# Kernel optimization log

Hardware: AMD Instinct MI355X
Metric: run time of the kernel (lower is better)

Reference implementation:

```python
import jax, jax.numpy as jnp
import numpy as np

N_MOL, E_MOL = 50000, 200000
N_PRO, E_PRO = 100000, 800000


def segment_softmax(e, seg, n):
    # e: [E, H] logits, softmax over edges grouped by target node `seg`
    m = jax.ops.segment_max(e, seg, num_segments=n)
    m = jnp.where(jnp.isfinite(m), m, jnp.zeros_like(m))
    ex = jnp.exp(e - m[seg])
    s = jax.ops.segment_sum(ex, seg, num_segments=n)
    return ex / (s[seg] + 1e-16)


def gat_conv(x, edge_index, W, a_src, a_dst, b, heads, out_ch):
    # torch_geometric GATConv (concat=True, add_self_loops=True, neg slope 0.2, eval mode)
    n = x.shape[0]
    loop = jnp.arange(n, dtype=edge_index.dtype)
    src = jnp.concatenate([edge_index[0], loop])
    dst = jnp.concatenate([edge_index[1], loop])
    h = (x @ W).reshape(n, heads, out_ch)            # [N,H,C]
    alpha_s = jnp.sum(h * a_src, axis=-1)            # [N,H]
    alpha_d = jnp.sum(h * a_dst, axis=-1)            # [N,H]
    e = jax.nn.leaky_relu(alpha_s[src] + alpha_d[dst], 0.2)  # [E,H]
    alpha = segment_softmax(e, dst, n)               # [E,H]
    out = jax.ops.segment_sum(alpha[:, :, None] * h[src], dst, num_segments=n)  # [N,H,C]
    return out.reshape(n, heads * out_ch) + b


def gcn_conv(x, edge_index, edge_weight, W, b):
    # torch_geometric GCNConv with edge_weight (add_self_loops=True, sym norm)
    n = x.shape[0]
    loop = jnp.arange(n, dtype=edge_index.dtype)
    src = jnp.concatenate([edge_index[0], loop])
    dst = jnp.concatenate([edge_index[1], loop])
    w = jnp.concatenate([edge_weight, jnp.ones((n,), x.dtype)])
    deg = jax.ops.segment_sum(w, dst, num_segments=n)
    dinv = jnp.where(deg > 0, deg ** -0.5, jnp.zeros_like(deg))
    norm = dinv[src] * w * dinv[dst]                 # [E]
    h = x @ W                                        # [N,C]
    return jax.ops.segment_sum(norm[:, None] * h[src], dst, num_segments=n) + b


def setup_inputs() -> dict:
    key = jax.random.key(0)
    ks = iter(jax.random.split(key, 32))
    rn = lambda shape, s=0.1: jax.random.normal(next(ks), shape, dtype=jnp.float32) * s
    inp = {
        "mol_x": rn((N_MOL, 78), 1.0),
        "mol_edge_index": jax.random.randint(next(ks), (2, E_MOL), 0, N_MOL, dtype=jnp.int32),
        "pro_x": rn((N_PRO, 33), 1.0),
        "pro_edge_index": jax.random.randint(next(ks), (2, E_PRO), 0, N_PRO, dtype=jnp.int32),
        "pro_edge_weight": jax.random.uniform(next(ks), (E_PRO,), dtype=jnp.float32),
        # mol_conv1: GAT 78->78, heads=2
        "W1": rn((78, 156)), "a_src1": rn((2, 78)), "a_dst1": rn((2, 78)), "b1": jnp.zeros((156,), jnp.float32),
        # mol_conv2: GAT 156->156, heads=2
        "W2": rn((156, 312)), "a_src2": rn((2, 156)), "a_dst2": rn((2, 156)), "b2": jnp.zeros((312,), jnp.float32),
        # mol_conv3: GAT 312->312, heads=1
        "W3": rn((312, 312)), "a_src3": rn((1, 312)), "a_dst3": rn((1, 312)), "b3": jnp.zeros((312,), jnp.float32),
        # pro_conv1: GCN 33->33
        "Wp1": rn((33, 33)), "bp1": jnp.zeros((33,), jnp.float32),
        # pro_conv2: GAT 33->66, heads=2
        "Wp2": rn((33, 132)), "ap_src2": rn((2, 66)), "ap_dst2": rn((2, 66)), "bp2": jnp.zeros((132,), jnp.float32),
        # pro_conv3: GAT 132->132, heads=1
        "Wp3": rn((132, 132)), "ap_src3": rn((1, 132)), "ap_dst3": rn((1, 132)), "bp3": jnp.zeros((132,), jnp.float32),
    }
    return inp


def reference(mol_x, mol_edge_index, pro_x, pro_edge_index, pro_edge_weight,
              W1, a_src1, a_dst1, b1, W2, a_src2, a_dst2, b2, W3, a_src3, a_dst3, b3,
              Wp1, bp1, Wp2, ap_src2, ap_dst2, bp2, Wp3, ap_src3, ap_dst3, bp3):
    # mol branch (per CPI_GAT.forward): conv1 -> relu -> conv2 -> relu -> conv3
    x = jax.nn.relu(gat_conv(mol_x, mol_edge_index, W1, a_src1, a_dst1, b1, 2, 78))
    x = jax.nn.relu(gat_conv(x, mol_edge_index, W2, a_src2, a_dst2, b2, 2, 156))
    x = gat_conv(x, mol_edge_index, W3, a_src3, a_dst3, b3, 1, 312)
    # pro branch: gcn -> relu -> gat -> relu -> gat -> relu
    xt = jax.nn.relu(gcn_conv(pro_x, pro_edge_index, pro_edge_weight, Wp1, bp1))
    xt = jax.nn.relu(gat_conv(xt, pro_edge_index, Wp2, ap_src2, ap_dst2, bp2, 2, 66))
    xt = jax.nn.relu(gat_conv(xt, pro_edge_index, Wp3, ap_src3, ap_dst3, bp3, 1, 132))
    return (x, xt)
```

## Files before the change

### kernel.cpp

```cpp
#include <hip/hip_runtime.h>
#include <cstdint>
#include <cstddef>

#define WAVE 64
#define NPB 4

#define TBM 128
#define TBN 128
#define TBK 32
#define LDK 40

typedef short s16x8 __attribute__((ext_vector_type(8)));
typedef float f32x4 __attribute__((ext_vector_type(4)));

__device__ __forceinline__ unsigned short f2bf(float f) {
    unsigned int u = __float_as_uint(f);
    unsigned int r = (u + 0x7fffu + ((u >> 16) & 1u)) >> 16;
    return (unsigned short)r;
}
__device__ __forceinline__ float bf2f_lo(unsigned int v) { return __uint_as_float(v << 16); }
__device__ __forceinline__ float bf2f_hi(unsigned int v) { return __uint_as_float(v & 0xffff0000u); }
__device__ __forceinline__ float lrelu02(float e) { return (e > 0.f) ? e : 0.2f * e; }


__device__ __forceinline__ void gemm_body(const unsigned short* __restrict__ A,
                                          const unsigned short* __restrict__ BT,
                                          unsigned short* __restrict__ Cbf,
                                          float* __restrict__ asb, float* __restrict__ adb,
                                          int N, int Kp, int M, int Mext, int Mp, int H,
                                          int bx, int by) {
    __shared__ __align__(16) unsigned short As[TBM * LDK];
    __shared__ __align__(16) unsigned short Bs[TBN * LDK];
    int tid = threadIdx.x;
    int wave = tid >> 6;
    int lane = tid & 63;
    int rowBase = by * TBM;
    int colBase = bx * TBN;
    int wm = (wave & 1) * 64;
    int wn = (wave >> 1) * 64;
    int l15 = lane & 15;
    int quad = lane >> 4;

    f32x4 acc[4][4];
    f32x4 z4 = {0.f, 0.f, 0.f, 0.f};
#pragma unroll
    for (int i = 0; i < 4; i++)
#pragma unroll
        for (int j = 0; j < 4; j++) acc[i][j] = z4;

    int srow = tid >> 2;
    int skg = tid & 3;
    const uint4 zero16 = {0u, 0u, 0u, 0u};

    for (int k0 = 0; k0 < Kp; k0 += TBK) {
#pragma unroll
        for (int half = 0; half < 2; half++) {
            int row = srow + half * 64;
            int gk = k0 + skg * 8;
            bool kok = (gk < Kp);
            {
                int gr = rowBase + row;
                uint4 v = zero16;
                if (kok && gr < N) v = *(const uint4*)(A + (size_t)gr * Kp + gk);
                *(uint4*)(As + row * LDK + skg * 8) = v;
            }
            {
                int gc = colBase + row;
                uint4 v = zero16;
                if (kok && gc < Mext) v = *(const uint4*)(BT + (size_t)gc * Kp + gk);
                *(uint4*)(Bs + row * LDK + skg * 8) = v;
            }
        }
        __syncthreads();

        s16x8 af[4], bfr[4];
#pragma unroll
        for (int mt = 0; mt < 4; mt++)
            af[mt] = *(const s16x8*)(As + (wm + mt * 16 + l15) * LDK + quad * 8);
#pragma unroll
        for (int nt = 0; nt < 4; nt++)
            bfr[nt] = *(const s16x8*)(Bs + (wn + nt * 16 + l15) * LDK + quad * 8);
#pragma unroll
        for (int mt = 0; mt < 4; mt++)
#pragma unroll
            for (int nt = 0; nt < 4; nt++)
                acc[mt][nt] = __builtin_amdgcn_mfma_f32_16x16x32_bf16(af[mt], bfr[nt], acc[mt][nt], 0, 0, 0);
        __syncthreads();
    }

#pragma unroll
    for (int mt = 0; mt < 4; mt++) {
#pragma unroll
        for (int r = 0; r < 4; r++) {
            int row = rowBase + wm + mt * 16 + quad * 4 + r;
            if (row < N) {
#pragma unroll
                for (int nt = 0; nt < 4; nt++) {
                    int col = colBase + wn + nt * 16 + l15;
                    float v = acc[mt][nt][r];
                    if (col < M) {
                        Cbf[(size_t)row * Mp + col] = f2bf(v);
                    } else if (asb != nullptr && col < M + 2 * H) {
                        int t = col - M;
                        if (t < H) asb[(size_t)row * H + t] = v;
                        else adb[(size_t)row * H + (t - H)] = v;
                    }
                }
            }
        }
    }
}


template <int SLOTS, int G, int H, bool SM, int SWEEPS, bool GCN>
__device__ __forceinline__ void agg_body(const unsigned short* __restrict__ hfeat,
                                         const float* __restrict__ as_, const float* __restrict__ ad_,
                                         const float* __restrict__ dinv,
                                         const int* __restrict__ rowp, const int2* __restrict__ cpack,
                                         const float* __restrict__ bias,
                                         float* __restrict__ out_f, unsigned short* __restrict__ out_bf,
                                         int HC, int ldo, int relu, int n, int lane) {
    constexpr int ROWB = SWEEPS * SLOTS * 16;
    int g = lane / SLOTS;
    int slot = lane - g * SLOTS;
    bool act = (g < G);
    int C = HC / H;
    int beg = rowp[n], end = rowp[n + 1];

    float adn[H], msub[H];
    float di = 0.f;
    if (GCN) {
        di = dinv[n];
    } else {
#pragma unroll
        for (int h = 0; h < H; h++) {
            adn[h] = ad_[(size_t)n * H + h];
            msub[h] = lrelu02(as_[(size_t)n * H + h] + adn[h]);
        }
    }

    int ch0[SWEEPS];
    bool h1q[SWEEPS][4];
#pragma unroll
    for (int sw = 0; sw < SWEEPS; sw++) {
        ch0[sw] = (sw * SLOTS + slot) * 8;
#pragma unroll
        for (int q = 0; q < 4; q++) h1q[sw][q] = (H == 2) && ((ch0[sw] + 2 * q) >= C);
    }

    float sfw = GCN ? di * di : 1.f;
    float accx[SWEEPS][4], accy[SWEEPS][4];
#pragma unroll
    for (int sw = 0; sw < SWEEPS; sw++)
#pragma unroll
        for (int q = 0; q < 4; q++) { accx[sw][q] = 0.f; accy[sw][q] = 0.f; }
    if (act && g == 0) {
#pragma unroll
        for (int sw = 0; sw < SWEEPS; sw++) {
            uint4 v = *(const uint4*)((const char*)hfeat + (size_t)n * ROWB + (sw * SLOTS + slot) * 16);
            unsigned int vv[4] = {v.x, v.y, v.z, v.w};
#pragma unroll
            for (int q = 0; q < 4; q++) { accx[sw][q] = sfw * bf2f_lo(vv[q]); accy[sw][q] = sfw * bf2f_hi(vv[q]); }
        }
    }

    float wsum[H];
#pragma unroll
    for (int h = 0; h < H; h++) wsum[h] = 0.f;

    for (int base = beg; base < end; base += WAVE) {
        int cnt = end - base;
        if (cnt > WAVE) cnt = WAVE;
        int s_l = 0;
// ... 80 lines not shown
                        unsigned int ub[4] = {vB[sw].x, vB[sw].y, vB[sw].z, vB[sw].w};
#pragma unroll
                        for (int q = 0; q < 4; q++) {
                            float wq = (H == 2) ? (h1q[sw][q] ? wB[1] : wB[0]) : wB[0];
                            accx[sw][q] += wq * bf2f_lo(ub[q]);
                            accy[sw][q] += wq * bf2f_hi(ub[q]);
                        }
                    }
                }
            }
        }
    }

    if (G == 3) {
#pragma unroll
        for (int sw = 0; sw < SWEEPS; sw++)
#pragma unroll
            for (int q = 0; q < 4; q++) {
                int b1a = (lane + SLOTS) << 2, b2a = (lane + 2 * SLOTS) << 2;
                float t1 = __uint_as_float((unsigned)__builtin_amdgcn_ds_bpermute(b1a, (int)__float_as_uint(accx[sw][q])));
                float t2 = __uint_as_float((unsigned)__builtin_amdgcn_ds_bpermute(b2a, (int)__float_as_uint(accx[sw][q])));
                accx[sw][q] += t1 + t2;
                float t3 = __uint_as_float((unsigned)__builtin_amdgcn_ds_bpermute(b1a, (int)__float_as_uint(accy[sw][q])));
                float t4 = __uint_as_float((unsigned)__builtin_amdgcn_ds_bpermute(b2a, (int)__float_as_uint(accy[sw][q])));
                accy[sw][q] += t3 + t4;
            }
    } else if (G == 8) {
#pragma unroll
        for (int st = 4; st >= 1; st >>= 1) {
            int ba = (lane + st * SLOTS) << 2;
#pragma unroll
            for (int sw = 0; sw < SWEEPS; sw++)
#pragma unroll
                for (int q = 0; q < 4; q++) {
                    accx[sw][q] += __uint_as_float((unsigned)__builtin_amdgcn_ds_bpermute(ba, (int)__float_as_uint(accx[sw][q])));
                    accy[sw][q] += __uint_as_float((unsigned)__builtin_amdgcn_ds_bpermute(ba, (int)__float_as_uint(accy[sw][q])));
                }
        }
    }

    float rs[H];
    if (SM) {
#pragma unroll
        for (int h = 0; h < H; h++) {
            float t = wsum[h];
            for (int off = 32; off > 0; off >>= 1) t += __shfl_xor(t, off);
            rs[h] = 1.f / (1.f + t + 1e-16f);
        }
    } else {
#pragma unroll
        for (int h = 0; h < H; h++) rs[h] = 1.f;
    }

    if (lane < SLOTS) {
#pragma unroll
        for (int sw = 0; sw < SWEEPS; sw++) {
            float o[8];
#pragma unroll
            for (int q = 0; q < 4; q++) {
                float r = (H == 2) ? (h1q[sw][q] ? rs[1] : rs[0]) : rs[0];
                int c0 = ch0[sw] + 2 * q;
                float b0 = (c0 < HC) ? bias[c0] : 0.f;
                float b1v = (c0 + 1 < HC) ? bias[c0 + 1] : 0.f;
                float o0 = accx[sw][q] * r + b0;
                float o1 = accy[sw][q] * r + b1v;
                if (relu) { o0 = fmaxf(o0, 0.f); o1 = fmaxf(o1, 0.f); }
                if (c0 >= HC) o0 = 0.f;
                if (c0 + 1 >= HC) o1 = 0.f;
                o[2 * q] = o0;
                o[2 * q + 1] = o1;
            }
            if (out_bf) {
                uint4 pk;
                unsigned* pp = (unsigned*)&pk;
#pragma unroll
                for (int q = 0; q < 4; q++)
                    pp[q] = (unsigned)f2bf(o[2 * q]) | ((unsigned)f2bf(o[2 * q + 1]) << 16);
                *(uint4*)((char*)out_bf + (size_t)n * ((size_t)ldo * 2) + (sw * SLOTS + slot) * 16) = pk;
            } else {
#pragma unroll
                for (int half = 0; half < 2; half++) {
                    int c0 = ch0[sw] + half * 4;
                    if (c0 < HC) {
                        float4 f4 = make_float4(o[half * 4], o[half * 4 + 1], o[half * 4 + 2], o[half * 4 + 3]);
                        *(float4*)(out_f + (size_t)n * HC + c0) = f4;
                    }
                }
            }
        }
    }
}


__device__ __forceinline__ void cvtw1(const float* __restrict__ W, unsigned short* __restrict__ WT,
                                      int K, int M, int Kp, int i) {
    int m = i / Kp;
    int k = i - m * Kp;
    WT[i] = (k < K) ? f2bf(W[(long long)k * M + m]) : (unsigned short)0;
}

__device__ __forceinline__ void prep1(const float* __restrict__ W, const float* __restrict__ a_src,
                                      const float* __restrict__ a_dst, unsigned short* __restrict__ WT,
                                      int K, int M, int C, int Kp, int H, int b, int lane) {
    int k = b % Kp;
    int th = b / Kp;
    int t = th / H;
    int h = th - t * H;
    size_t orow = (size_t)(M + t * H + h) * Kp;
    if (k >= K) {
        if (lane == 0) WT[orow + k] = 0;
        return;
    }
    const float* a = t ? a_dst : a_src;
    int hoff = h * C;
    const float* wrow = W + (size_t)k * M + hoff;
    float acc = 0.f;
    for (int c = lane; c < C; c += 64) acc += wrow[c] * a[hoff + c];
    for (int off = 32; off > 0; off >>= 1) acc += __shfl_down(acc, off);
    if (lane == 0) WT[orow + k] = f2bf(acc);
}


__global__ __launch_bounds__(256) void k_A(
    const int* __restrict__ mol_dst, const int* __restrict__ pro_dst, int* __restrict__ cnt,
    int N_MOL, int E_MOL, int ET, int nb1,
    const float* __restrict__ W1, const float* __restrict__ W2, const float* __restrict__ W3,
    const float* __restrict__ Wp1, const float* __restrict__ Wp2, const float* __restrict__ Wp3,
    unsigned short* __restrict__ wt1, unsigned short* __restrict__ wt2, unsigned short* __restrict__ wt3,
    unsigned short* __restrict__ wtp1, unsigned short* __restrict__ wtp2, unsigned short* __restrict__ wtp3,
    const float* __restrict__ as1, const float* __restrict__ ad1,
    const float* __restrict__ as2, const float* __restrict__ ad2,
    const float* __restrict__ as3, const float* __restrict__ ad3,
    const float* __restrict__ aps2, const float* __restrict__ apd2,
    const float* __restrict__ aps3, const float* __restrict__ apd3,
    const float* __restrict__ mol_x, unsigned short* __restrict__ xb,
    const float* __restrict__ pro_x, unsigned short* __restrict__ xpp,
    long long totM, long long totP) {
    const int nb2 = 730;
    const int nb3 = 508;
    int b = blockIdx.x;
    int tid = threadIdx.x;
    if (b < nb1) {
        int i0 = b * 1024 + tid;
#pragma unroll
        for (int k = 0; k < 4; k++) {
            int e = i0 + k * 256;
            if (e < ET) {
                int d = (e < E_MOL) ? mol_dst[e] : (N_MOL + pro_dst[e - E_MOL]);
                atomicAdd(&cnt[d], 1);
            }
        }
    } else if (b < nb1 + nb2) {
        int idx = (b - nb1) * 256 + tid;
        if (idx < 12480)        cvtw1(W1, wt1, 78, 156, 80, idx);
        else if (idx < 62400)   cvtw1(W2, wt2, 156, 312, 160, idx - 12480);
        else if (idx < 162240)  cvtw1(W3, wt3, 312, 312, 320, idx - 62400);
        else if (idx < 163560)  cvtw1(Wp1, wtp1, 33, 33, 40, idx - 162240);
        else if (idx < 168840)  cvtw1(Wp2, wtp2, 33, 132, 40, idx - 163560);
        else if (idx < 186792)  cvtw1(Wp3, wtp3, 132, 132, 136, idx - 168840);
    } else if (b < nb1 + nb2 + nb3) {
        int unit = (b - nb1 - nb2) * 4 + (tid >> 6);
        int lane = tid & 63;
        if (unit < 320)        prep1(W1, as1, ad1, wt1, 78, 156, 78, 80, 2, unit, lane);
        else if (unit < 960)   prep1(W2, as2, ad2, wt2, 156, 312, 156, 160, 2, unit - 320, lane);
        else if (unit < 1600)  prep1(W3, as3, ad3, wt3, 312, 312, 312, 320, 1, unit - 960, lane);
        else if (unit < 1760)  prep1(Wp2, aps2, apd2, wtp2, 33, 132, 66, 40, 2, unit - 1600, lane);
        else if (unit < 2032)  prep1(Wp3, aps3, apd3, wtp3, 132, 132, 132, 136, 1, unit - 1760, lane);
    } else {
        long long i0 = (long long)(b - nb1 - nb2 - nb3) * 1024 + tid;
#pragma unroll
        for (int k = 0; k < 4; k++) {
            long long idx = i0 + k * 256;
            if (idx < totM) {
                int n = (int)(idx / 80);
                int kk = (int)(idx - (long long)n * 80);
                xb[idx] = (kk < 78) ? f2bf(mol_x[(long long)n * 78 + kk]) : (unsigned short)0;
            } else if (idx < totM + totP) {
                long long i2 = idx - totM;
                int n = (int)(i2 / 40);
                int kk = (int)(i2 - (long long)n * 40);
                xpp[i2] = (kk < 33) ? f2bf(pro_x[(long long)n * 33 + kk]) : (unsigned short)0;
            }
        }
    }
}


__global__ __launch_bounds__(256) void k_scan1(const int* __restrict__ cnt, int* __restrict__ incl,
                                               int* __restrict__ bsums, int n) {
    __shared__ int sm[256];
    int i = blockIdx.x * 256 + threadIdx.x;
    int v = (i < n) ? cnt[i] : 0;
    sm[threadIdx.x] = v;
    __syncthreads();
    for (int off = 1; off < 256; off <<= 1) {
        int t = (threadIdx.x >= off) ? sm[threadIdx.x - off] : 0;
        __syncthreads();
        sm[threadIdx.x] += t;
        __syncthreads();
    }
    if (i < n) incl[i] = sm[threadIdx.x];
    if (threadIdx.x == 255) bsums[blockIdx.x] = sm[255];
}

__global__ __launch_bounds__(1024) void k_scan2(int* __restrict__ bsums, int nb) {
    __shared__ int sm[1024];
    int v = (threadIdx.x < nb) ? bsums[threadIdx.x] : 0;
    sm[threadIdx.x] = v;
    __syncthreads();
    for (int off = 1; off < 1024; off <<= 1) {
        int t = (threadIdx.x >= off) ? sm[threadIdx.x - off] : 0;
        __syncthreads();
        sm[threadIdx.x] += t;
        __syncthreads();
    }
    if (threadIdx.x < nb) bsums[threadIdx.x] = sm[threadIdx.x] - v;
}

__global__ __launch_bounds__(256) void k_scan3_all(const int* __restrict__ incl, const int* __restrict__ cnt,
                                                   const int* __restrict__ boff,
                                                   int* __restrict__ mol_rowp, int* __restrict__ pro_rowp,
                                                   int* __restrict__ cur,
                                                   int N_MOL, int N_PRO, int E_MOL, int E_PRO) {
    int i = blockIdx.x * 256 + threadIdx.x;
    int NT = N_MOL + N_PRO;
    if (i < NT) {
        int ex = incl[i] - cnt[i] + boff[blockIdx.x];
        cur[i] = ex;
        if (i < N_MOL) mol_rowp[i] = ex;
        else pro_rowp[i - N_MOL] = ex - E_MOL;
    }
    if (i == 0) {
        mol_rowp[N_MOL] = E_MOL;
        pro_rowp[N_PRO] = E_PRO;
    }
}


__global__ __launch_bounds__(256) void k_B(
    const int* __restrict__ msrc, const int* __restrict__ mdst,
    const int* __restrict__ psrc, const int* __restrict__ pdst,
    const float* __restrict__ pw, int* __restrict__ cur, int2* __restrict__ cpack,
    int N_MOL, int E_MOL, int ET, int nbs,
    const unsigned short* __restrict__ A1, const unsigned short* __restrict__ B1,
    unsigned short* __restrict__ C1, float* __restrict__ as1o, float* __restrict__ ad1o,
    int N1, int Kp1, int M1, int Mext1, int Mp1, int H1, int g1x, int nb1,
    const unsigned short* __restrict__ A2, const unsigned short* __restrict__ B2,
    unsigned short* __restrict__ C2, float* __restrict__ as2o, float* __restrict__ ad2o,
    int N2, int Kp2, int M2, int Mext2, int Mp2, int H2, int g2x) {
    int b = blockIdx.x;
    if (b < nbs) {
        int e = b * 256 + threadIdx.x;
        if (e < ET) {
            int s, d;
            int wbits = 0;
            if (e >= E_MOL) {
                int ep = e - E_MOL;
                s = psrc[ep];
                d = N_MOL + pdst[ep];
                wbits = __float_as_int(pw[ep]);
            } else {
                s = msrc[e];
                d = mdst[e];
            }
            int pos = atomicAdd(&cur[d], 1);
            int2 pk;
            pk.x = s;
            pk.y = wbits;
            cpack[pos] = pk;
        }
    } else if (b < nbs + nb1) {
        int bb = b - nbs;
        gemm_body(A1, B1, C1, as1o, ad1o, N1, Kp1, M1, Mext1, Mp1, H1, bb % g1x, bb / g1x);
    } else {
        int bb = b - nbs - nb1;
        gemm_body(A2, B2, C2, as2o, ad2o, N2, Kp2, M2, Mext2, Mp2, H2, bb % g2x, bb / g2x);
    }
}


__global__ __launch_bounds__(256) void k_deg(const int* __restrict__ rowp, const int2* __restrict__ cpack,
                                             float* __restrict__ dinv, int N) {
    int n = blockIdx.x * 256 + threadIdx.x;
    if (n < N) {
        int b = rowp[n], e = rowp[n + 1];
        float s = 0.f;
        for (int p = b; p < e; p++) s += __int_as_float(cpack[p].y);
        dinv[n] = rsqrtf(s + 1.0f);
    }
}


__global__ __launch_bounds__(NPB * 64) void k_fuse1(
    const unsigned short* __restrict__ hb, const float* __restrict__ asm_, const float* __restrict__ adm_,
    const int* __restrict__ mrowp, const int2* __restrict__ mcp, const float* __restrict__ b1,
    unsigned short* __restrict__ xb, int Nm,
    const unsigned short* __restrict__ hbp, const float* __restrict__ dinv,
    const int* __restrict__ prowp, const int2* __restrict__ pcp, const float* __restrict__ bp1,
    unsigned short* __restrict__ xpp, int Np, int nb1) {
    int wave = threadIdx.x >> 6, lane = threadIdx.x & 63;
    int b = blockIdx.x;
    if (b < nb1) {
        int n = b * NPB + wave;
        if (n < Nm)
            agg_body<20, 3, 2, true, 1, false>(hb, asm_, adm_, nullptr, mrowp, mcp, b1,
                                               nullptr, xb, 156, 160, 1, n, lane);
    } else {
        int n = (b - nb1) * NPB + wave;
        if (n < Np)
            agg_body<5, 8, 1, false, 1, true>(hbp, nullptr, nullptr, dinv, prowp, pcp, bp1,
                                              nullptr, xpp, 33, 40, 1, n, lane);
    }
}

__global__ __launch_bounds__(NPB * 64) void k_fuse3(
    const unsigned short* __restrict__ hb, const float* __restrict__ asm_, const float* __restrict__ adm_,
    const int* __restrict__ mrowp, const int2* __restrict__ mcp, const float* __restrict__ b2,
    unsigned short* __restrict__ xb, int Nm,
    const unsigned short* __restrict__ hbp, const float* __restrict__ asp_, const float* __restrict__ adp_,
    const int* __restrict__ prowp, const int2* __restrict__ pcp, const float* __restrict__ bp2,
    unsigned short* __restrict__ xpp, int Np, int nb1) {
    int wave = threadIdx.x >> 6, lane = threadIdx.x & 63;
    int b = blockIdx.x;
    if (b < nb1) {
        int n = b * NPB + wave;
        if (n < Nm)
            agg_body<20, 3, 2, true, 2, false>(hb, asm_, adm_, nullptr, mrowp, mcp, b2,
                                               nullptr, xb, 312, 320, 1, n, lane);
    } else {
        int n = (b - nb1) * NPB + wave;
        if (n < Np)
            agg_body<17, 3, 2, true, 1, false>(hbp, asp_, adp_, nullptr, prowp, pcp, bp2,
                                               nullptr, xpp, 132, 136, 1, n, lane);
    }
}

__global__ __launch_bounds__(NPB * 64) void k_fuse5(
    const unsigned short* __restrict__ hb, const float* __restrict__ asm_, const float* __restrict__ adm_,
    const int* __restrict__ mrowp, const int2* __restrict__ mcp, const float* __restrict__ b3,
    float* __restrict__ out_mol, int Nm,
    const unsigned short* __restrict__ hbp, const float* __restrict__ asp_, const float* __restrict__ adp_,
    const int* __restrict__ prowp, const int2* __restrict__ pcp, const float* __restrict__ bp3,
    float* __restrict__ out_pro, int Np, int nb1) {
    int wave = threadIdx.x >> 6, lane = threadIdx.x & 63;
    int b = blockIdx.x;
    if (b < nb1) {
        int n = b * NPB + wave;
        if (n < Nm)
            agg_body<20, 3, 1, true, 2, false>(hb, asm_, adm_, nullptr, mrowp, mcp, b3,
                                               out_mol, nullptr, 312, 320, 0, n, lane);
    } else {
        int n = (b - nb1) * NPB + wave;
        if (n < Np)
            agg_body<17, 3, 1, true, 1, false>(hbp, asp_, adp_, nullptr, prowp, pcp, bp3,
                                               out_pro, nullptr, 132, 136, 1, n, lane);
    }
}


extern "C" void kernel_launch(void* const* d_in, const int* in_sizes, int n_in,
                              void* d_out, int out_size, void* d_ws, size_t ws_size,
                              hipStream_t stream) {
    const int N_MOL = in_sizes[0] / 78;
    const int E_MOL = in_sizes[1] / 2;
    const int N_PRO = in_sizes[2] / 33;
    const int E_PRO = in_sizes[3] / 2;
    const int NT = N_MOL + N_PRO;
    const int ET = E_MOL + E_PRO;

    const float* mol_x = (const float*)d_in[0];
    const int* mol_ei = (const int*)d_in[1];
    const float* pro_x = (const float*)d_in[2];
    const int* pro_ei = (const int*)d_in[3];
    const float* pro_ew = (const float*)d_in[4];
    const float *W1 = (const float*)d_in[5], *as1 = (const float*)d_in[6], *ad1 = (const float*)d_in[7],
                *b1 = (const float*)d_in[8];
    const float *W2 = (const float*)d_in[9], *as2 = (const float*)d_in[10], *ad2 = (const float*)d_in[11],
                *b2 = (const float*)d_in[12];
    const float *W3 = (const float*)d_in[13], *as3 = (const float*)d_in[14], *ad3 = (const float*)d_in[15],
                *b3 = (const float*)d_in[16];
    const float *Wp1 = (const float*)d_in[17], *bp1 = (const float*)d_in[18];
    const float *Wp2 = (const float*)d_in[19], *aps2 = (const float*)d_in[20], *apd2 = (const float*)d_in[21],
                *bp2 = (const float*)d_in[22];
    const float *Wp3 = (const float*)d_in[23], *aps3 = (const float*)d_in[24], *apd3 = (const float*)d_in[25],
                *bp3 = (const float*)d_in[26];

    float* out_mol = (float*)d_out;
    float* out_pro = (float*)d_out + (size_t)N_MOL * 312;

    char* p = (char*)d_ws;
    auto alloc = [&](size_t bytes) -> void* {
        void* r = (void*)p;
        p += (bytes + 255) & ~(size_t)255;
        return r;
    };
    int* cnt_all  = (int*)alloc((size_t)NT * 4);
    int* incl     = (int*)alloc((size_t)NT * 4);
    int* cur_all  = (int*)alloc((size_t)NT * 4);
    int* bsums    = (int*)alloc(1024 * 4);
    int* mol_rowp = (int*)alloc((size_t)(N_MOL + 1) * 4);
    int* pro_rowp = (int*)alloc((size_t)(N_PRO + 1) * 4);
    int2* cpack   = (int2*)alloc((size_t)ET * 8);
    float* dinv   = (float*)alloc((size_t)N_PRO * 4);
    float* asb_m = (float*)alloc((size_t)N_MOL * 2 * 4);
    float* adb_m = (float*)alloc((size_t)N_MOL * 2 * 4);
    float* asb_p = (float*)alloc((size_t)N_PRO * 2 * 4);
    float* adb_p = (float*)alloc((size_t)N_PRO * 2 * 4);
    unsigned short* hb  = (unsigned short*)alloc((size_t)N_MOL * 320 * 2);
    unsigned short* xb  = (unsigned short*)alloc((size_t)N_MOL * 320 * 2);
    unsigned short* hbp = (unsigned short*)alloc((size_t)N_PRO * 136 * 2);
    unsigned short* xpp = (unsigned short*)alloc((size_t)N_PRO * 136 * 2);
    unsigned short* wt1 = (unsigned short*)alloc((size_t)160 * 80 * 2);
    unsigned short* wt2 = (unsigned short*)alloc((size_t)320 * 160 * 2);
    unsigned short* wt3 = (unsigned short*)alloc((size_t)320 * 320 * 2);
    unsigned short* wtp1 = (unsigned short*)alloc((size_t)40 * 40 * 2);
    unsigned short* wtp2 = (unsigned short*)alloc((size_t)136 * 40 * 2);
    unsigned short* wtp3 = (unsigned short*)alloc((size_t)136 * 136 * 2);
    (void)ws_size;

    int2* mol_cp = cpack;
    int2* pro_cp = cpack + E_MOL;

    const int* mol_src = mol_ei;
    const int* mol_dst = mol_ei + E_MOL;
    const int* pro_src = pro_ei;
    const int* pro_dst = pro_ei + E_PRO;

    const long long totM = (long long)N_MOL * 80;
    const long long totP = (long long)N_PRO * 40;

    hipMemsetAsync(cnt_all, 0, (size_t)NT * 4, stream);
    int nbCnt = (ET + 1023) / 1024;
    int nbCvx = (int)((totM + totP + 1023) / 1024);
    int gridA = nbCnt + 730 + 508 + nbCvx;
    k_A<<<gridA, 256, 0, stream>>>(mol_dst, pro_dst, cnt_all, N_MOL, E_MOL, ET, nbCnt,
                                   W1, W2, W3, Wp1, Wp2, Wp3, wt1, wt2, wt3, wtp1, wtp2, wtp3,
                                   as1, ad1, as2, ad2, as3, ad3, aps2, apd2, aps3, apd3,
                                   mol_x, xb, pro_x, xpp, totM, totP);

    int nbT = (NT + 255) / 256;
    k_scan1<<<nbT, 256, 0, stream>>>(cnt_all, incl, bsums, NT);
    k_scan2<<<1, 1024, 0, stream>>>(bsums, nbT);
    k_scan3_all<<<nbT, 256, 0, stream>>>(incl, cnt_all, bsums, mol_rowp, pro_rowp, cur_all,
                                         N_MOL, N_PRO, E_MOL, E_PRO);

    int gyM = (N_MOL + TBM - 1) / TBM;
    int gyP = (N_PRO + TBM - 1) / TBM;

    {
        int nbs = (ET + 255) / 256;
        int g1x = (160 + TBN - 1) / TBN;
        int nb1 = g1x * gyM;
        int g2x = 1;
        int nb2 = g2x * gyP;
        k_B<<<nbs + nb1 + nb2, 256, 0, stream>>>(
            mol_src, mol_dst, pro_src, pro_dst, pro_ew, cur_all, cpack, N_MOL, E_MOL, ET, nbs,
            xb, wt1, hb, asb_m, adb_m, N_MOL, 80, 156, 160, 160, 2, g1x, nb1,
            xpp, wtp1, hbp, nullptr, nullptr, N_PRO, 40, 33, 33, 40, 0, g2x);
    }

    k_deg<<<(N_PRO + 255) / 256, 256, 0, stream>>>(pro_rowp, pro_cp, dinv, N_PRO);

    {
        int nb1 = (N_MOL + NPB - 1) / NPB;
        int nb2 = (N_PRO + NPB - 1) / NPB;
        k_fuse1<<<nb1 + nb2, NPB * 64, 0, stream>>>(hb, asb_m, adb_m, mol_rowp, mol_cp, b1, xb, N_MOL,
                                                    hbp, dinv, pro_rowp, pro_cp, bp1, xpp, N_PRO, nb1);
    }

    {
        int g1x = (316 + TBN - 1) / TBN;
        int nb1 = g1x * gyM;
        int g2x = (136 + TBN - 1) / TBN;
        int nb2 = g2x * gyP;
        k_B<<<nb1 + nb2, 256, 0, stream>>>(
            nullptr, nullptr, nullptr, nullptr, nullptr, nullptr, nullptr, N_MOL, E_MOL, ET, 0,
            xb, wt2, hb, asb_m, adb_m, N_MOL, 160, 312, 316, 320, 2, g1x, nb1,
            xpp, wtp2, hbp, asb_p, adb_p, N_PRO, 40, 132, 136, 136, 2, g2x);
    }

    {
        int nb1 = (N_MOL + NPB - 1) / NPB;
        int nb2 = (N_PRO + NPB - 1) / NPB;
        k_fuse3<<<nb1 + nb2, NPB * 64, 0, stream>>>(hb, asb_m, adb_m, mol_rowp, mol_cp, b2, xb, N_MOL,
                                                    hbp, asb_p, adb_p, pro_rowp, pro_cp, bp2, xpp, N_PRO, nb1);
    }

    {
        int g1x = (314 + TBN - 1) / TBN;
        int nb1 = g1x * gyM;
        int g2x = (134 + TBN - 1) / TBN;
        int nb2 = g2x * gyP;
        k_B<<<nb1 + nb2, 256, 0, stream>>>(
            nullptr, nullptr, nullptr, nullptr, nullptr, nullptr, nullptr, N_MOL, E_MOL, ET, 0,
            xb, wt3, hb, asb_m, adb_m, N_MOL, 320, 312, 314, 320, 1, g1x, nb1,
            xpp, wtp3, hbp, asb_p, adb_p, N_PRO, 136, 132, 134, 136, 1, g2x);
    }

    {
        int nb1 = (N_MOL + NPB - 1) / NPB;
        int nb2 = (N_PRO + NPB - 1) / NPB;
        k_fuse5<<<nb1 + nb2, NPB * 64, 0, stream>>>(hb, asb_m, adb_m, mol_rowp, mol_cp, b3, out_mol, N_MOL,
                                                    hbp, asb_p, adb_p, pro_rowp, pro_cp, bp3, out_pro, N_PRO, nb1);
    }
}
```

Before: 764.7 us.

## Aggregate before transform for layer-2 GAT using block-diagonal weights

```diff
diff --git a/kernel.cpp b/kernel.cpp
--- a/kernel.cpp
+++ b/kernel.cpp
@@ -27,6 +27,7 @@
                                           const unsigned short* __restrict__ BT,
                                           unsigned short* __restrict__ Cbf,
                                           float* __restrict__ asb, float* __restrict__ adb,
+                                          const float* __restrict__ bias, int relu, int zpadTo,
                                           int N, int Kp, int M, int Mext, int Mp, int H,
                                           int bx, int by) {
     __shared__ __align__(16) unsigned short As[TBM * LDK];
@@ -99,7 +100,14 @@
                     int col = colBase + wn + nt * 16 + l15;
                     float v = acc[mt][nt][r];
                     if (col < M) {
-                        Cbf[(size_t)row * Mp + col] = f2bf(v);
+                        float v2 = v;
+                        if (bias != nullptr) {
+                            v2 += bias[col];
+                            if (relu) v2 = fmaxf(v2, 0.f);
+                        }
+                        Cbf[(size_t)row * Mp + col] = f2bf(v2);
+                    } else if (col < zpadTo) {
+                        Cbf[(size_t)row * Mp + col] = 0;
                     } else if (asb != nullptr && col < M + 2 * H) {
                         int t = col - M;
                         if (t < H) asb[(size_t)row * H + t] = v;
@@ -112,13 +120,15 @@
 }
 
 
-template <int SLOTS, int G, int H, bool SM, int SWEEPS, bool GCN>
+template <int SLOTS, int G, int H, bool SM, int SWEEPS, bool GCN, bool NEXTA>
 __device__ __forceinline__ void agg_body(const unsigned short* __restrict__ hfeat,
                                          const float* __restrict__ as_, const float* __restrict__ ad_,
                                          const float* __restrict__ dinv,
                                          const int* __restrict__ rowp, const int2* __restrict__ cpack,
                                          const float* __restrict__ bias,
                                          float* __restrict__ out_f, unsigned short* __restrict__ out_bf,
+                                         const float* __restrict__ vanf, int vald,
+                                         float* __restrict__ asn, float* __restrict__ adn_o,
                                          int HC, int ldo, int relu, int n, int lane) {
     constexpr int ROWB = SWEEPS * SLOTS * 16;
     int g = lane / SLOTS;
@@ -305,6 +315,7 @@
         for (int h = 0; h < H; h++) rs[h] = 1.f;
     }
 
+    float ps[4] = {0.f, 0.f, 0.f, 0.f};
     if (lane < SLOTS) {
 #pragma unroll
         for (int sw = 0; sw < SWEEPS; sw++) {
@@ -323,6 +334,14 @@
                 o[2 * q] = o0;
                 o[2 * q + 1] = o1;
             }
+            if (NEXTA) {
+#pragma unroll
+                for (int j = 0; j < 8; j++) {
+                    int c = ch0[sw] + j;
+#pragma unroll
+                    for (int th = 0; th < 4; th++) ps[th] += o[j] * vanf[th * vald + c];
+                }
+            }
             if (out_bf) {
                 uint4 pk;
                 unsigned* pp = (unsigned*)&pk;
@@ -342,6 +361,175 @@
             }
         }
     }
+    if (NEXTA) {
+#pragma unroll
+        for (int th = 0; th < 4; th++)
+            for (int off = 32; off > 0; off >>= 1) ps[th] += __shfl_xor(ps[th], off);
+        if (lane == 0) {
+            asn[(size_t)n * 2 + 0] = ps[0];
+            asn[(size_t)n * 2 + 1] = ps[1];
+            adn_o[(size_t)n * 2 + 0] = ps[2];
+            adn_o[(size_t)n * 2 + 1] = ps[3];
+        }
+    }
+}
+
+
+template <int SLOTS, int G>
+__device__ __forceinline__ void aggN_body(const unsigned short* __restrict__ x,
+                                          const float* __restrict__ as_, const float* __restrict__ ad_,
+                                          const int* __restrict__ rowp, const int2* __restrict__ cpack,
+                                          unsigned short* __restrict__ A2, int n, int lane) {
+    constexpr int ROWB = SLOTS * 16;
+    int g = lane / SLOTS;
+    int slot = lane - g * SLOTS;
+    bool act = (g < G);
+    int beg = rowp[n], end = rowp[n + 1];
+
+    float adn[2], msub[2];
+#pragma unroll
+    for (int h = 0; h < 2; h++) {
+        adn[h] = ad_[(size_t)n * 2 + h];
+        msub[h] = lrelu02(as_[(size_t)n * 2 + h] + adn[h]);
+    }
+
+    float ax[2][4], ay[2][4];
+#pragma unroll
+    for (int h = 0; h < 2; h++)
+#pragma unroll
+        for (int q = 0; q < 4; q++) { ax[h][q] = 0.f; ay[h][q] = 0.f; }
+    if (act && g == 0) {
+        uint4 v = *(const uint4*)((const char*)x + (size_t)n * ROWB + slot * 16);
+        unsigned int vv[4] = {v.x, v.y, v.z, v.w};
+#pragma unroll
+        for (int q = 0; q < 4; q++) {
+            float lo = bf2f_lo(vv[q]), hi = bf2f_hi(vv[q]);
+            ax[0][q] = lo; ax[1][q] = lo;
+            ay[0][q] = hi; ay[1][q] = hi;
+        }
+    }
+
+    float wsum[2] = {0.f, 0.f};
+
+    for (int base = beg; base < end; base += WAVE) {
+        int cnt = end - base;
+        if (cnt > WAVE) cnt = WAVE;
+        int s_l = 0;
+        float w_l[2] = {0.f, 0.f};
+        if (lane < cnt) {
+            s_l = cpack[base + lane].x;
+#pragma unroll
+            for (int h = 0; h < 2; h++)
+                w_l[h] = __expf(lrelu02(as_[(size_t)s_l * 2 + h] + adn[h]) - msub[h]);
+            wsum[0] += w_l[0];
+            wsum[1] += w_l[1];
+        }
+        for (int j0 = 0; j0 < cnt; j0 += 2 * G) {
+            int sA;
+            float wA[2];
+            uint4 vA;
+            {
+                int jj = j0 + g;
+                bool pad = (jj >= cnt);
+                if (jj > cnt - 1) jj = cnt - 1;
+                int ba = jj << 2;
+                sA = __builtin_amdgcn_ds_bpermute(ba, s_l);
+#pragma unroll
+                for (int h = 0; h < 2; h++) {
+                    float t = __uint_as_float(
+                        (unsigned)__builtin_amdgcn_ds_bpermute(ba, (int)__float_as_uint(w_l[h])));
+                    wA[h] = pad ? 0.f : t;
+                }
+                if (act) vA = *(const uint4*)((const char*)x + (unsigned)sA * ROWB + slot * 16);
+            }
+            bool haveB = (j0 + G < cnt);
+            int sB;
+            float wB[2];
+            uint4 vB;
+            if (haveB) {
+                int jj = j0 + G + g;
+                bool pad = (jj >= cnt);
+                if (jj > cnt - 1) jj = cnt - 1;
+                int ba = jj << 2;
+                sB = __builtin_amdgcn_ds_bpermute(ba, s_l);
+#pragma unroll
+                for (int h = 0; h < 2; h++) {
+                    float t = __uint_as_float(
+                        (unsigned)__builtin_amdgcn_ds_bpermute(ba, (int)__float_as_uint(w_l[h])));
+                    wB[h] = pad ? 0.f : t;
+                }
+                if (act) vB = *(const uint4*)((const char*)x + (unsigned)sB * ROWB + slot * 16);
+            }
+            if (act) {
+                unsigned int va[4] = {vA.x, vA.y, vA.z, vA.w};
+#pragma unroll
+                for (int q = 0; q < 4; q++) {
+                    float lo = bf2f_lo(va[q]), hi = bf2f_hi(va[q]);
+                    ax[0][q] += wA[0] * lo; ax[1][q] += wA[1] * lo;
+                    ay[0][q] += wA[0] * hi; ay[1][q] += wA[1] * hi;
+                }
+                if (haveB) {
+                    unsigned int ub[4] = {vB.x, vB.y, vB.z, vB.w};
+#pragma unroll
+                    for (int q = 0; q < 4; q++) {
+                        float lo = bf2f_lo(ub[q]), hi = bf2f_hi(ub[q]);
+                        ax[0][q] += wB[0] * lo; ax[1][q] += wB[1] * lo;
+                        ay[0][q] += wB[0] * hi; ay[1][q] += wB[1] * hi;
+                    }
+                }
+            }
+        }
+    }
+
+    if (G == 3) {
+#pragma unroll
+        for (int h = 0; h < 2; h++)
+#pragma unroll
+            for (int q = 0; q < 4; q++) {
+                int b1a = (lane + SLOTS) << 2, b2a = (lane + 2 * SLOTS) << 2;
+                float t1 = __uint_as_float((unsigned)__builtin_amdgcn_ds_bpermute(b1a, (int)__float_as_uint(ax[h][q])));
+                float t2 = __uint_as_float((unsigned)__builtin_amdgcn_ds_bpermute(b2a, (int)__float_as_uint(ax[h][q])));
+                ax[h][q] += t1 + t2;
+                float t3 = __uint_as_float((unsigned)__builtin_amdgcn_ds_bpermute(b1a, (int)__float_as_uint(ay[h][q])));
+                float t4 = __uint_as_float((unsigned)__builtin_amdgcn_ds_bpermute(b2a, (int)__float_as_uint(ay[h][q])));
+                ay[h][q] += t3 + t4;
+            }
+    } else if (G == 8) {
+#pragma unroll
+        for (int st = 4; st >= 1; st >>= 1) {
+            int ba = (lane + st * SLOTS) << 2;
+#pragma unroll
+            for (int h = 0; h < 2; h++)
+#pragma unroll
+                for (int q = 0; q < 4; q++) {
+                    ax[h][q] += __uint_as_float((unsigned)__builtin_amdgcn_ds_bpermute(ba, (int)__float_as_uint(ax[h][q])));
+                    ay[h][q] += __uint_as_float((unsigned)__builtin_amdgcn_ds_bpermute(ba, (int)__float_as_uint(ay[h][q])));
+                }
+        }
+    }
+
+    float rs[2];
+#pragma unroll
+    for (int h = 0; h < 2; h++) {
+        float t = wsum[h];
+        for (int off = 32; off > 0; off >>= 1) t += __shfl_xor(t, off);
+        rs[h] = 1.f / (1.f + t + 1e-16f);
+    }
+
+    if (lane < SLOTS) {
+#pragma unroll
+        for (int h = 0; h < 2; h++) {
+            uint4 pk;
+            unsigned* pp = (unsigned*)&pk;
+#pragma unroll
+            for (int q = 0; q < 4; q++) {
+                float o0 = ax[h][q] * rs[h];
+                float o1 = ay[h][q] * rs[h];
+                pp[q] = (unsigned)f2bf(o0) | ((unsigned)f2bf(o1) << 16);
+            }
+            *(uint4*)((char*)A2 + (size_t)n * (2 * ROWB) + h * ROWB + slot * 16) = pk;
+        }
+    }
 }
 
 
@@ -350,6 +538,19 @@
     int m = i / Kp;
     int k = i - m * Kp;
     WT[i] = (k < K) ? f2bf(W[(long long)k * M + m]) : (unsigned short)0;
+}
+
+__device__ __forceinline__ void cvtw_bd(const float* __restrict__ W, unsigned short* __restrict__ WT,
+                                        int K, int M, int C, int Kp, int Kph, int i) {
+    int m = i / Kp;
+    int k = i - m * Kp;
+    unsigned short v = 0;
+    if (m < M) {
+        int hm = m / C;
+        int kk = k - hm * Kph;
+        if (kk >= 0 && kk < K) v = f2bf(W[(long long)kk * M + m]);
+    }
+    WT[i] = v;
 }
 
 __device__ __forceinline__ void prep1(const float* __restrict__ W, const float* __restrict__ a_src,
@@ -373,23 +574,44 @@
     if (lane == 0) WT[orow + k] = f2bf(acc);
 }
 
+__device__ __forceinline__ void prep1f(const float* __restrict__ W, const float* __restrict__ a_src,
+                                       const float* __restrict__ a_dst, float* __restrict__ fout,
+                                       int K, int M, int C, int Kp, int H, int b, int lane) {
+    int k = b % Kp;
+    int th = b / Kp;
+    int t = th / H;
+    int h = th - t * H;
+    if (k >= K) {
+        if (lane == 0) fout[(size_t)th * Kp + k] = 0.f;
+        return;
+    }
+    const float* a = t ? a_dst : a_src;
+    int hoff = h * C;
+    const float* wrow = W + (size_t)k * M + hoff;
+    float acc = 0.f;
+    for (int c = lane; c < C; c += 64) acc += wrow[c] * a[hoff + c];
+    for (int off = 32; off > 0; off >>= 1) acc += __shfl_down(acc, off);
+    if (lane == 0) fout[(size_t)th * Kp + k] = acc;
+}
+
 
 __global__ __launch_bounds__(256) void k_A(
     const int* __restrict__ mol_dst, const int* __restrict__ pro_dst, int* __restrict__ cnt,
     int N_MOL, int E_MOL, int ET, int nb1,
     const float* __restrict__ W1, const float* __restrict__ W2, const float* __restrict__ W3,
     const float* __restrict__ Wp1, const float* __restrict__ Wp2, const float* __restrict__ Wp3,
-    unsigned short* __restrict__ wt1, unsigned short* __restrict__ wt2, unsigned short* __restrict__ wt3,
-    unsigned short* __restrict__ wtp1, unsigned short* __restrict__ wtp2, unsigned short* __restrict__ wtp3,
+    unsigned short* __restrict__ wt1, unsigned short* __restrict__ wt2bd, unsigned short* __restrict__ wt3,
+    unsigned short* __restrict__ wtp1, unsigned short* __restrict__ wtp2bd, unsigned short* __restrict__ wtp3,
     const float* __restrict__ as1, const float* __restrict__ ad1,
     const float* __restrict__ as2, const float* __restrict__ ad2,
     const float* __restrict__ as3, const float* __restrict__ ad3,
     const float* __restrict__ aps2, const float* __restrict__ apd2,
     const float* __restrict__ aps3, const float* __restrict__ apd3,
+    float* __restrict__ va2f, float* __restrict__ vap2f,
     const float* __restrict__ mol_x, unsigned short* __restrict__ xb,
     const float* __restrict__ pro_x, unsigned short* __restrict__ xpp,
     long long totM, long long totP) {
-    const int nb2 = 730;
+    const int nb2 = 957;
     const int nb3 = 508;
     int b = blockIdx.x;
     int tid = threadIdx.x;
@@ -406,18 +628,18 @@
     } else if (b < nb1 + nb2) {
         int idx = (b - nb1) * 256 + tid;
         if (idx < 12480)        cvtw1(W1, wt1, 78, 156, 80, idx);
-        else if (idx < 62400)   cvtw1(W2, wt2, 156, 312, 160, idx - 12480);
-        else if (idx < 162240)  cvtw1(W3, wt3, 312, 312, 320, idx - 62400);
-        else if (idx < 163560)  cvtw1(Wp1, wtp1, 33, 33, 40, idx - 162240);
-        else if (idx < 168840)  cvtw1(Wp2, wtp2, 33, 132, 40, idx - 163560);
-        else if (idx < 186792)  cvtw1(Wp3, wtp3, 132, 132, 136, idx - 168840);
+        else if (idx < 114880)  cvtw_bd(W2, wt2bd, 156, 312, 156, 320, 160, idx - 12480);
+        else if (idx < 214720)  cvtw1(W3, wt3, 312, 312, 320, idx - 114880);
+        else if (idx < 216040)  cvtw1(Wp1, wtp1, 33, 33, 40, idx - 214720);
+        else if (idx < 226920)  cvtw_bd(Wp2, wtp2bd, 33, 132, 66, 80, 40, idx - 216040);
+        else if (idx < 244872)  cvtw1(Wp3, wtp3, 132, 132, 136, idx - 226920);
     } else if (b < nb1 + nb2 + nb3) {
         int unit = (b - nb1 - nb2) * 4 + (tid >> 6);
         int lane = tid & 63;
         if (unit < 320)        prep1(W1, as1, ad1, wt1, 78, 156, 78, 80, 2, unit, lane);
-        else if (unit < 960)   prep1(W2, as2, ad2, wt2, 156, 312, 156, 160, 2, unit - 320, lane);
+        else if (unit < 960)   prep1f(W2, as2, ad2, va2f, 156, 312, 156, 160, 2, unit - 320, lane);
         else if (unit < 1600)  prep1(W3, as3, ad3, wt3, 312, 312, 312, 320, 1, unit - 960, lane);
-        else if (unit < 1760)  prep1(Wp2, aps2, apd2, wtp2, 33, 132, 66, 40, 2, unit - 1600, lane);
+        else if (unit < 1760)  prep1f(Wp2, aps2, apd2, vap2f, 33, 132, 66, 40, 2, unit - 1600, lane);
         else if (unit < 2032)  prep1(Wp3, aps3, apd3, wtp3, 132, 132, 132, 136, 1, unit - 1760, lane);
     } else {
         long long i0 = (long long)(b - nb1 - nb2 - nb3) * 1024 + tid;
@@ -497,9 +719,11 @@
     int N_MOL, int E_MOL, int ET, int nbs,
     const unsigned short* __restrict__ A1, const unsigned short* __restrict__ B1,
     unsigned short* __restrict__ C1, float* __restrict__ as1o, float* __restrict__ ad1o,
+    const float* __restrict__ bias1, int relu1, int zpad1,
     int N1, int Kp1, int M1, int Mext1, int Mp1, int H1, int g1x, int nb1,
     const unsigned short* __restrict__ A2, const unsigned short* __restrict__ B2,
     unsigned short* __restrict__ C2, float* __restrict__ as2o, float* __restrict__ ad2o,
+    const float* __restrict__ bias2, int relu2, int zpad2,
     int N2, int Kp2, int M2, int Mext2, int Mp2, int H2, int g2x) {
     int b = blockIdx.x;
     if (b < nbs) {
@@ -524,10 +748,10 @@
         }
     } else if (b < nbs + nb1) {
         int bb = b - nbs;
-        gemm_body(A1, B1, C1, as1o, ad1o, N1, Kp1, M1, Mext1, Mp1, H1, bb % g1x, bb / g1x);
+        gemm_body(A1, B1, C1, as1o, ad1o, bias1, relu1, zpad1, N1, Kp1, M1, Mext1, Mp1, H1, bb % g1x, bb / g1x);
     } else {
         int bb = b - nbs - nb1;
-        gemm_body(A2, B2, C2, as2o, ad2o, N2, Kp2, M2, Mext2, Mp2, H2, bb % g2x, bb / g2x);
+        gemm_body(A2, B2, C2, as2o, ad2o, bias2, relu2, zpad2, N2, Kp2, M2, Mext2, Mp2, H2, bb % g2x, bb / g2x);
     }
 }
 
@@ -547,44 +771,43 @@
 __global__ __launch_bounds__(NPB * 64) void k_fuse1(
     const unsigned short* __restrict__ hb, const float* __restrict__ asm_, const float* __restrict__ adm_,
     const int* __restrict__ mrowp, const int2* __restrict__ mcp, const float* __restrict__ b1,
-    unsigned short* __restrict__ xb, int Nm,
+    unsigned short* __restrict__ x2m, const float* __restrict__ va2f,
+    float* __restrict__ asm2, float* __restrict__ adm2, int Nm,
     const unsigned short* __restrict__ hbp, const float* __restrict__ dinv,
     const int* __restrict__ prowp, const int2* __restrict__ pcp, const float* __restrict__ bp1,
-    unsigned short* __restrict__ xpp, int Np, int nb1) {
+    unsigned short* __restrict__ x2p, const float* __restrict__ vap2f,
+    float* __restrict__ asp2, float* __restrict__ adp2, int Np, int nb1) {
     int wave = threadIdx.x >> 6, lane = threadIdx.x & 63;
     int b = blockIdx.x;
     if (b < nb1) {
         int n = b * NPB + wave;
         if (n < Nm)
-            agg_body<20, 3, 2, true, 1, false>(hb, asm_, adm_, nullptr, mrowp, mcp, b1,
-                                               nullptr, xb, 156, 160, 1, n, lane);
+            agg_body<20, 3, 2, true, 1, false, true>(hb, asm_, adm_, nullptr, mrowp, mcp, b1,
+                                                     nullptr, x2m, va2f, 160, asm2, adm2,
+                                                     156, 160, 1, n, lane);
     } else {
         int n = (b - nb1) * NPB + wave;
         if (n < Np)
-            agg_body<5, 8, 1, false, 1, true>(hbp, nullptr, nullptr, dinv, prowp, pcp, bp1,
-                                              nullptr, xpp, 33, 40, 1, n, lane);
-    }
-}
-
-__global__ __launch_bounds__(NPB * 64) void k_fuse3(
-    const unsigned short* __restrict__ hb, const float* __restrict__ asm_, const float* __restrict__ adm_,
-    const int* __restrict__ mrowp, const int2* __restrict__ mcp, const float* __restrict__ b2,
-    unsigned short* __restrict__ xb, int Nm,
-    const unsigned short* __restrict__ hbp, const float* __restrict__ asp_, const float* __restrict__ adp_,
-    const int* __restrict__ prowp, const int2* __restrict__ pcp, const float* __restrict__ bp2,
-    unsigned short* __restrict__ xpp, int Np, int nb1) {
+            agg_body<5, 8, 1, false, 1, true, true>(hbp, nullptr, nullptr, dinv, prowp, pcp, bp1,
+                                                    nullptr, x2p, vap2f, 40, asp2, adp2,
+                                                    33, 40, 1, n, lane);
+    }
+}
+
+__global__ __launch_bounds__(NPB * 64) void k_fuseN(
+    const unsigned short* __restrict__ x2m, const float* __restrict__ asm2, const float* __restrict__ adm2,
+    const int* __restrict__ mrowp, const int2* __restrict__ mcp, unsigned short* __restrict__ xa2m, int Nm,
+    const unsigned short* __restrict__ x2p, const float* __restrict__ asp2, const float* __restrict__ adp2,
+    const int* __restrict__ prowp, const int2* __restrict__ pcp, unsigned short* __restrict__ xa2p, int Np,
+    int nb1) {
     int wave = threadIdx.x >> 6, lane = threadIdx.x & 63;
     int b = blockIdx.x;
     if (b < nb1) {
         int n = b * NPB + wave;
-        if (n < Nm)
-            agg_body<20, 3, 2, true, 2, false>(hb, asm_, adm_, nullptr, mrowp, mcp, b2,
-                                               nullptr, xb, 312, 320, 1, n, lane);
+        if (n < Nm) aggN_body<20, 3>(x2m, asm2, adm2, mrowp, mcp, xa2m, n, lane);
     } else {
         int n = (b - nb1) * NPB + wave;
-        if (n < Np)
-            agg_body<17, 3, 2, true, 1, false>(hbp, asp_, adp_, nullptr, prowp, pcp, bp2,
-                                               nullptr, xpp, 132, 136, 1, n, lane);
+        if (n < Np) aggN_body<5, 8>(x2p, asp2, adp2, prowp, pcp, xa2p, n, lane);
     }
 }
 
@@ -600,13 +823,15 @@
     if (b < nb1) {
         int n = b * NPB + wave;
         if (n < Nm)
-            agg_body<20, 3, 1, true, 2, false>(hb, asm_, adm_, nullptr, mrowp, mcp, b3,
-                                               out_mol, nullptr, 312, 320, 0, n, lane);
+            agg_body<20, 3, 1, true, 2, false, false>(hb, asm_, adm_, nullptr, mrowp, mcp, b3,
+                                                      out_mol, nullptr, nullptr, 0, nullptr, nullptr,
+                                                      312, 320, 0, n, lane);
     } else {
         int n = (b - nb1) * NPB + wave;
         if (n < Np)
-            agg_body<17, 3, 1, true, 1, false>(hbp, asp_, adp_, nullptr, prowp, pcp, bp3,
-                                               out_pro, nullptr, 132, 136, 1, n, lane);
+            agg_body<17, 3, 1, true, 1, false, false>(hbp, asp_, adp_, nullptr, prowp, pcp, bp3,
+                                                      out_pro, nullptr, nullptr, 0, nullptr, nullptr,
+                                                      132, 136, 1, n, lane);
     }
 }
 
@@ -641,6 +866,18 @@
     float* out_mol = (float*)d_out;
     float* out_pro = (float*)d_out + (size_t)N_MOL * 312;
 
+    char* ob = (char*)d_out;
+    size_t o_xa2m = 0;
+    size_t o_xa2p = o_xa2m + (size_t)N_MOL * 320 * 2;
+    size_t o_xb0  = o_xa2p + (size_t)N_PRO * 80 * 2;
+    size_t o_xp0  = o_xb0 + (size_t)N_MOL * 80 * 2;
+    size_t o_xpp  = o_xp0 + (size_t)N_PRO * 40 * 2;
+    unsigned short* xa2m = (unsigned short*)(ob + o_xa2m);
+    unsigned short* xa2p = (unsigned short*)(ob + o_xa2p);
+    unsigned short* xb0  = (unsigned short*)(ob + o_xb0);
+    unsigned short* xp0  = (unsigned short*)(ob + o_xp0);
+    unsigned short* xpp  = (unsigned short*)(ob + o_xpp);
+
     char* p = (char*)d_ws;
     auto alloc = [&](size_t bytes) -> void* {
         void* r = (void*)p;
@@ -655,21 +892,34 @@
     int* pro_rowp = (int*)alloc((size_t)(N_PRO + 1) * 4);
     int2* cpack   = (int2*)alloc((size_t)ET * 8);
     float* dinv   = (float*)alloc((size_t)N_PRO * 4);
-    float* asb_m = (float*)alloc((size_t)N_MOL * 2 * 4);
-    float* adb_m = (float*)alloc((size_t)N_MOL * 2 * 4);
-    float* asb_p = (float*)alloc((size_t)N_PRO * 2 * 4);
-    float* adb_p = (float*)alloc((size_t)N_PRO * 2 * 4);
-    unsigned short* hb  = (unsigned short*)alloc((size_t)N_MOL * 320 * 2);
-    unsigned short* xb  = (unsigned short*)alloc((size_t)N_MOL * 320 * 2);
-    unsigned short* hbp = (unsigned short*)alloc((size_t)N_PRO * 136 * 2);
-    unsigned short* xpp = (unsigned short*)alloc((size_t)N_PRO * 136 * 2);
-    unsigned short* wt1 = (unsigned short*)alloc((size_t)160 * 80 * 2);
-    unsigned short* wt2 = (unsigned short*)alloc((size_t)320 * 160 * 2);
-    unsigned short* wt3 = (unsigned short*)alloc((size_t)320 * 320 * 2);
-    unsigned short* wtp1 = (unsigned short*)alloc((size_t)40 * 40 * 2);
-    unsigned short* wtp2 = (unsigned short*)alloc((size_t)136 * 40 * 2);
-    unsigned short* wtp3 = (unsigned short*)alloc((size_t)136 * 136 * 2);
+    float* asb_m  = (float*)alloc((size_t)N_MOL * 2 * 4);
+    float* adb_m  = (float*)alloc((size_t)N_MOL * 2 * 4);
+    float* asb_m2 = (float*)alloc((size_t)N_MOL * 2 * 4);
+    float* adb_m2 = (float*)alloc((size_t)N_MOL * 2 * 4);
+    float* asb_p  = (float*)alloc((size_t)N_PRO * 2 * 4);
+    float* adb_p  = (float*)alloc((size_t)N_PRO * 2 * 4);
+    float* asb_p2 = (float*)alloc((size_t)N_PRO * 2 * 4);
+    float* adb_p2 = (float*)alloc((size_t)N_PRO * 2 * 4);
+    float* va2f   = (float*)alloc((size_t)4 * 160 * 4);
+    float* vap2f  = (float*)alloc((size_t)4 * 40 * 4);
+    unsigned short* bufA = (unsigned short*)alloc((size_t)N_MOL * 320 * 2);
+    unsigned short* bufB = (unsigned short*)alloc((size_t)N_MOL * 320 * 2);
+    unsigned short* bufC = (unsigned short*)alloc((size_t)N_PRO * 136 * 2);
+    unsigned short* wt1    = (unsigned short*)alloc((size_t)160 * 80 * 2);
+    unsigned short* wt2bd  = (unsigned short*)alloc((size_t)320 * 320 * 2);
+    unsigned short* wt3    = (unsigned short*)alloc((size_t)320 * 320 * 2);
+    unsigned short* wtp1   = (unsigned short*)alloc((size_t)40 * 40 * 2);
+    unsigned short* wtp2bd = (unsigned short*)alloc((size_t)136 * 80 * 2);
+    unsigned short* wtp3   = (unsigned short*)alloc((size_t)136 * 136 * 2);
     (void)ws_size;
+
+    unsigned short* hb1  = bufA;
+    unsigned short* x3m  = bufA;
+    unsigned short* x2m  = bufB;
+    unsigned short* x2p  = bufB + (size_t)N_MOL * 160;
+    unsigned short* hb3  = bufB;
+    unsigned short* hbp1 = bufC;
+    unsigned short* hbp3 = bufC;
 
     int2* mol_cp = cpack;
     int2* pro_cp = cpack + E_MOL;
@@ -685,11 +935,11 @@
     hipMemsetAsync(cnt_all, 0, (size_t)NT * 4, stream);
     int nbCnt = (ET + 1023) / 1024;
     int nbCvx = (int)((totM + totP + 1023) / 1024);
-    int gridA = nbCnt + 730 + 508 + nbCvx;
+    int gridA = nbCnt + 957 + 508 + nbCvx;
     k_A<<<gridA, 256, 0, stream>>>(mol_dst, pro_dst, cnt_all, N_MOL, E_MOL, ET, nbCnt,
-                                   W1, W2, W3, Wp1, Wp2, Wp3, wt1, wt2, wt3, wtp1, wtp2, wtp3,
+                                   W1, W2, W3, Wp1, Wp2, Wp3, wt1, wt2bd, wt3, wtp1, wtp2bd, wtp3,
                                    as1, ad1, as2, ad2, as3, ad3, aps2, apd2, aps3, apd3,
-                                   mol_x, xb, pro_x, xpp, totM, totP);
+                                   va2f, vap2f, mol_x, xb0, pro_x, xp0, totM, totP);
 
     int nbT = (NT + 255) / 256;
     k_scan1<<<nbT, 256, 0, stream>>>(cnt_all, incl, bsums, NT);
@@ -702,14 +952,13 @@
 
     {
         int nbs = (ET + 255) / 256;
-        int g1x = (160 + TBN - 1) / TBN;
+        int g1x = 2;
         int nb1 = g1x * gyM;
         int g2x = 1;
-        int nb2 = g2x * gyP;
-        k_B<<<nbs + nb1 + nb2, 256, 0, stream>>>(
+        k_B<<<nbs + nb1 + g2x * gyP, 256, 0, stream>>>(
             mol_src, mol_dst, pro_src, pro_dst, pro_ew, cur_all, cpack, N_MOL, E_MOL, ET, nbs,
-            xb, wt1, hb, asb_m, adb_m, N_MOL, 80, 156, 160, 160, 2, g1x, nb1,
-            xpp, wtp1, hbp, nullptr, nullptr, N_PRO, 40, 33, 33, 40, 0, g2x);
+            xb0, wt1, hb1, asb_m, adb_m, nullptr, 0, 0, N_MOL, 80, 156, 160, 160, 2, g1x, nb1,
+            xp0, wtp1, hbp1, nullptr, nullptr, nullptr, 0, 0, N_PRO, 40, 33, 33, 40, 0, g2x);
     }
 
     k_deg<<<(N_PRO + 255) / 256, 256, 0, stream>>>(pro_rowp, pro_cp, dinv, N_PRO);
@@ -717,43 +966,43 @@
     {
         int nb1 = (N_MOL + NPB - 1) / NPB;
         int nb2 = (N_PRO + NPB - 1) / NPB;
-        k_fuse1<<<nb1 + nb2, NPB * 64, 0, stream>>>(hb, asb_m, adb_m, mol_rowp, mol_cp, b1, xb, N_MOL,
-                                                    hbp, dinv, pro_rowp, pro_cp, bp1, xpp, N_PRO, nb1);
-    }
-
-    {
-        int g1x = (316 + TBN - 1) / TBN;
-        int nb1 = g1x * gyM;
-        int g2x = (136 + TBN - 1) / TBN;
-        int nb2 = g2x * gyP;
-        k_B<<<nb1 + nb2, 256, 0, stream>>>(
-            nullptr, nullptr, nullptr, nullptr, nullptr, nullptr, nullptr, N_MOL, E_MOL, ET, 0,
-            xb, wt2, hb, asb_m, adb_m, N_MOL, 160, 312, 316, 320, 2, g1x, nb1,
-            xpp, wtp2, hbp, asb_p, adb_p, N_PRO, 40, 132, 136, 136, 2, g2x);
+        k_fuse1<<<nb1 + nb2, NPB * 64, 0, stream>>>(hb1, asb_m, adb_m, mol_rowp, mol_cp, b1,
+                                                    x2m, va2f, asb_m2, adb_m2, N_MOL,
+                                                    hbp1, dinv, pro_rowp, pro_cp, bp1,
+                                                    x2p, vap2f, asb_p2, adb_p2, N_PRO, nb1);
     }
 
     {
         int nb1 = (N_MOL + NPB - 1) / NPB;
         int nb2 = (N_PRO + NPB - 1) / NPB;
-        k_fuse3<<<nb1 + nb2, NPB * 64, 0, stream>>>(hb, asb_m, adb_m, mol_rowp, mol_cp, b2, xb, N_MOL,
-                                                    hbp, asb_p, adb_p, pro_rowp, pro_cp, bp2, xpp, N_PRO, nb1);
+        k_fuseN<<<nb1 + nb2, NPB * 64, 0, stream>>>(x2m, asb_m2, adb_m2, mol_rowp, mol_cp, xa2m, N_MOL,
+                                                    x2p, asb_p2, adb_p2, pro_rowp, pro_cp, xa2p, N_PRO, nb1);
     }
 
     {
-        int g1x = (314 + TBN - 1) / TBN;
+        int g1x = 3;
         int nb1 = g1x * gyM;
-        int g2x = (134 + TBN - 1) / TBN;
-        int nb2 = g2x * gyP;
-        k_B<<<nb1 + nb2, 256, 0, stream>>>(
+        int g2x = 2;
+        k_B<<<nb1 + g2x * gyP, 256, 0, stream>>>(
             nullptr, nullptr, nullptr, nullptr, nullptr, nullptr, nullptr, N_MOL, E_MOL, ET, 0,
-            xb, wt3, hb, asb_m, adb_m, N_MOL, 320, 312, 314, 320, 1, g1x, nb1,
-            xpp, wtp3, hbp, asb_p, adb_p, N_PRO, 136, 132, 134, 136, 1, g2x);
+            xa2m, wt2bd, x3m, nullptr, nullptr, b2, 1, 320, N_MOL, 320, 312, 320, 320, 0, g1x, nb1,
+            xa2p, wtp2bd, xpp, nullptr, nullptr, bp2, 1, 136, N_PRO, 80, 132, 136, 136, 0, g2x);
+    }
+
+    {
+        int g1x = 3;
+        int nb1 = g1x * gyM;
+        int g2x = 2;
+        k_B<<<nb1 + g2x * gyP, 256, 0, stream>>>(
+            nullptr, nullptr, nullptr, nullptr, nullptr, nullptr, nullptr, N_MOL, E_MOL, ET, 0,
+            x3m, wt3, hb3, asb_m, adb_m, nullptr, 0, 0, N_MOL, 320, 312, 314, 320, 1, g1x, nb1,
+            xpp, wtp3, hbp3, asb_p, adb_p, nullptr, 0, 0, N_PRO, 136, 132, 134, 136, 1, g2x);
     }
 
     {
         int nb1 = (N_MOL + NPB - 1) / NPB;
         int nb2 = (N_PRO + NPB - 1) / NPB;
-        k_fuse5<<<nb1 + nb2, NPB * 64, 0, stream>>>(hb, asb_m, adb_m, mol_rowp, mol_cp, b3, out_mol, N_MOL,
-                                                    hbp, asb_p, adb_p, pro_rowp, pro_cp, bp3, out_pro, N_PRO, nb1);
-    }
-}
+        k_fuse5<<<nb1 + nb2, NPB * 64, 0, stream>>>(hb3, asb_m, adb_m, mol_rowp, mol_cp, b3, out_mol, N_MOL,
+                                                    hbp3, asb_p, adb_p, pro_rowp, pro_cp, bp3, out_pro, N_PRO, nb1);
+    }
+}
```

After: 842.6 us. 10.2% more time.
